# Optimization experiments

Measured on AMD Instinct MI355X. Metric: run time of the kernel, lower is better.

## Reference

```python
import jax, jax.numpy as jnp
import numpy as np

# ---- config (from Mamba2Config defaults) ----
D_MODEL = 1024
D_STATE = 128
D_CONV = 4
EXPAND = 2
HEADDIM = 64
D_INNER = EXPAND * D_MODEL          # 2048
NHEADS = D_INNER // HEADDIM         # 32
CONV_DIM = D_INNER + 2 * D_STATE    # 2304 (ngroups=1)
D_IN_PROJ = 2 * D_INNER + 2 * D_STATE + NHEADS  # 4384
INTER = ((int(D_MODEL * 8 / 3) + 63) // 64) * 64  # 2752
EPS = 1e-6
BATCH, SEQLEN = 2, 1024


def rmsnorm(x, w):
    return x * jax.lax.rsqrt(jnp.mean(x * x, axis=-1, keepdims=True) + EPS) * w


def setup_inputs() -> dict:
    key = jax.random.key(0)
    ks = jax.random.split(key, 16)
    s = 0.02
    return {
        "hidden_states": jax.random.normal(ks[0], (BATCH, SEQLEN, D_MODEL), jnp.float32),
        "norm_w": jnp.ones((D_MODEL,), jnp.float32),
        "in_proj_w": jax.random.normal(ks[1], (D_IN_PROJ, D_MODEL), jnp.float32) * s,
        "conv_w": jax.random.normal(ks[2], (CONV_DIM, D_CONV), jnp.float32) * 0.2,
        "conv_b": jnp.zeros((CONV_DIM,), jnp.float32),
        "dt_bias": jax.random.normal(ks[3], (NHEADS,), jnp.float32) * 0.5,
        "A_log": jnp.log(jax.random.uniform(ks[4], (NHEADS,), jnp.float32, 1.0, 16.0)),
        "D": jnp.ones((NHEADS,), jnp.float32) + jax.random.normal(ks[5], (NHEADS,), jnp.float32) * 0.05,
        "ssm_norm_w": jnp.ones((D_INNER,), jnp.float32),
        "out_proj_w": jax.random.normal(ks[6], (D_MODEL, D_INNER), jnp.float32) * s,
        "post_norm_w": jnp.ones((D_MODEL,), jnp.float32),
        "gate_w": jax.random.normal(ks[7], (INTER, D_MODEL), jnp.float32) * s,
        "up_w": jax.random.normal(ks[8], (INTER, D_MODEL), jnp.float32) * s,
        "down_w": jax.random.normal(ks[9], (D_MODEL, INTER), jnp.float32) * s,
    }


def _mixer(u, in_proj_w, conv_w, conv_b, dt_bias, A_log, D, ssm_norm_w, out_proj_w):
    b, l, _ = u.shape
    zxbcdt = u @ in_proj_w.T                              # (b,l,4384)
    z = zxbcdt[..., :D_INNER]                             # gate
    xBC = zxbcdt[..., D_INNER:D_INNER + CONV_DIM]
    dt = zxbcdt[..., -NHEADS:]

    # causal depthwise conv1d (kernel D_CONV) + SiLU
    xp = jnp.pad(xBC, ((0, 0), (D_CONV - 1, 0), (0, 0)))
    xBC = sum(xp[:, k:k + l, :] * conv_w[:, k] for k in range(D_CONV)) + conv_b
    xBC = jax.nn.silu(xBC)

    xs = xBC[..., :D_INNER].reshape(b, l, NHEADS, HEADDIM)   # (b,l,h,p)
    Bm = xBC[..., D_INNER:D_INNER + D_STATE]                  # (b,l,n)
    Cm = xBC[..., -D_STATE:]                                  # (b,l,n)

    dt = jax.nn.softplus(dt + dt_bias)                        # (b,l,h)
    A = -jnp.exp(A_log)                                       # (h,)

    def step(h, inp):
        dt_t, x_t, B_t, C_t = inp                             # (b,h),(b,h,p),(b,n),(b,n)
        dA = jnp.exp(dt_t * A)                                # (b,h)
        h = h * dA[..., None, None] + jnp.einsum('bh,bhp,bn->bhpn', dt_t, x_t, B_t)
        y_t = jnp.einsum('bhpn,bn->bhp', h, C_t)
        return h, y_t

    h0 = jnp.zeros((b, NHEADS, HEADDIM, D_STATE), u.dtype)
    xsT = (jnp.moveaxis(dt, 1, 0), jnp.moveaxis(xs, 1, 0),
           jnp.moveaxis(Bm, 1, 0), jnp.moveaxis(Cm, 1, 0))
    _, yT = jax.lax.scan(step, h0, xsT)                       # (l,b,h,p)
    y = jnp.moveaxis(yT, 0, 1) + D[None, None, :, None] * xs  # skip term
    y = y.reshape(b, l, D_INNER)

    # gated RMSNorm (norm_before_gate=False): normalize y*silu(z)
    y = rmsnorm(y * jax.nn.silu(z), ssm_norm_w)
    return y @ out_proj_w.T


def reference(hidden_states, norm_w, in_proj_w, conv_w, conv_b, dt_bias, A_log, D,
              ssm_norm_w, out_proj_w, post_norm_w, gate_w, up_w, down_w):
    res = hidden_states
    h = rmsnorm(hidden_states, norm_w)
    h = _mixer(h, in_proj_w, conv_w, conv_b, dt_bias, A_log, D, ssm_norm_w, out_proj_w)
    x = res + h
    res = x
    h = rmsnorm(x, post_norm_w)
    h = (jax.nn.silu(h @ gate_w.T) * (h @ up_w.T)) @ down_w.T  # SwiGLU MLP
    return res + h
```

## Files before the change

### kernel.cpp

```cpp
#include <hip/hip_runtime.h>
#include <hip/hip_bf16.h>

#define SEQLEN   1024
#define NTOK     2048
#define DMODEL   1024
#define DSTATE   128
#define DINNER   2048
#define NHEADS   32
#define HEADDIM  64
#define CONVDIM  2304
#define DINPROJ  4384
#define INTER    2752
#define Q        64
#define NCHUNK   16

typedef __hip_bfloat16 bf16;
typedef unsigned short ushort_t;
typedef __attribute__((ext_vector_type(8))) short bf16x8;
typedef __attribute__((ext_vector_type(4))) float f32x4;
typedef __attribute__((ext_vector_type(4))) unsigned short u16x4;

__device__ __forceinline__ float bf2f(bf16 x) { return __bfloat162float(x); }
__device__ __forceinline__ float bfu2f(ushort_t u) {
    return __uint_as_float(((unsigned)u) << 16);
}
__device__ __forceinline__ ushort_t f2bfu(float x) {
    union { bf16 h; ushort_t u; } c; c.h = __float2bfloat16(x); return c.u;
}

__device__ __forceinline__ void glds16(const void* g, void* l) {
    __builtin_amdgcn_global_load_lds(
        (const __attribute__((address_space(1))) void*)g,
        (__attribute__((address_space(3))) void*)l, 16, 0, 0);
}

__device__ inline float block_reduce_sum(float v) {
    __shared__ float red[4];
    #pragma unroll
    for (int off = 32; off >= 1; off >>= 1) v += __shfl_down(v, off);
    int lane = threadIdx.x & 63, w = threadIdx.x >> 6;
    if (lane == 0) red[w] = v;
    __syncthreads();
    return red[0] + red[1] + red[2] + red[3];
}

__global__ __launch_bounds__(256) void f2bf_kernel(
    const float* __restrict__ src, ushort_t* __restrict__ dst, int n)
{
    const int i = (blockIdx.x * 256 + threadIdx.x) * 4;
    if (i < n) {
        const f32x4 v = *(const f32x4*)(src + i);
        u16x4 o;
        #pragma unroll
        for (int k = 0; k < 4; k++) o[k] = f2bfu(v[k]);
        *(u16x4*)(dst + i) = o;
    }
}

#define NWOP (DMODEL * DINNER)
#define NWG  (INTER * DMODEL)
__global__ __launch_bounds__(256) void convert_weights_kernel(
    const float* __restrict__ wop, const float* __restrict__ wg,
    const float* __restrict__ wu, const float* __restrict__ wd,
    ushort_t* __restrict__ dWop, ushort_t* __restrict__ dWgu,
    ushort_t* __restrict__ dWdn)
{
    const int i4 = (blockIdx.x * 256 + threadIdx.x) * 4;
    const float* src;
    ushort_t* dst;
    if (i4 < NWOP) { src = wop + i4; dst = dWop + i4; }
    else if (i4 < NWOP + NWG) {
        const int e = i4 - NWOP, row = e >> 10, col = e & 1023;
        src = wg + e; dst = dWgu + ((size_t)(2 * row) << 10) + col;
    } else if (i4 < NWOP + 2 * NWG) {
        const int e = i4 - NWOP - NWG, row = e >> 10, col = e & 1023;
        src = wu + e; dst = dWgu + ((size_t)(2 * row + 1) << 10) + col;
    } else if (i4 < NWOP + 3 * NWG) {
        const int e = i4 - NWOP - 2 * NWG;
        src = wd + e; dst = dWdn + e;
    } else return;
    const f32x4 v = *(const f32x4*)src;
    u16x4 o;
    #pragma unroll
    for (int k = 0; k < 4; k++) o[k] = f2bfu(v[k]);
    *(u16x4*)dst = o;
}

__global__ __launch_bounds__(256) void rmsnorm1024_kernel(
    const float* __restrict__ x, const float* __restrict__ w, bf16* __restrict__ out)
{
    const int token = blockIdx.x, t = threadIdx.x;
    float v[4]; float ss = 0.f;
    #pragma unroll
    for (int i = 0; i < 4; i++) {
        v[i] = x[(size_t)token * DMODEL + t * 4 + i];
        ss += v[i] * v[i];
    }
    ss = block_reduce_sum(ss);
    const float scale = rsqrtf(ss * (1.0f / DMODEL) + 1e-6f);
    #pragma unroll
    for (int i = 0; i < 4; i++)
        out[(size_t)token * DMODEL + t * 4 + i] =
            __float2bfloat16(v[i] * scale * w[t * 4 + i]);
}

template <int EPI, int MT, int NT>
__global__ __launch_bounds__(256) void gemm_bf(
    const bf16* __restrict__ A, const bf16* __restrict__ W,
    float* __restrict__ Cf, const float* __restrict__ resid_f,
    bf16* __restrict__ out_bf, int M, int N, int K)
{
    __shared__ ushort_t As[MT * 32];
    __shared__ ushort_t Bs[NT * 32];
    const int tid = threadIdx.x;
    const int w = tid >> 6, lane = tid & 63;
    const int m0 = blockIdx.y * MT, n0 = blockIdx.x * NT;

    const int srow = tid >> 2;
    const int skof = (tid & 3) * 8;
    const bf16* Ag0 = A + (size_t)(m0 + srow) * K + skof;
    const bf16* Ag1 = Ag0 + (size_t)64 * K;
    const int nr0 = n0 + srow, nr1 = n0 + 64 + srow;
    const bf16* Wg0 = W + (size_t)(nr0 < N ? nr0 : 0) * K + skof;
    const bf16* Wg1 = W + (size_t)((NT == 128 && nr1 < N) ? nr1 : 0) * K + skof;
    ushort_t* lA0 = &As[w * 512];
    ushort_t* lA1 = &As[2048 + w * 512];
    ushort_t* lB0 = &Bs[w * 512];
    ushort_t* lB1 = &Bs[2048 + w * 512];

    const int wy = w >> 1, wx = w & 1;
    const int fr = lane & 15;
    const int fk = (lane >> 4) * 8;
    constexpr int MI = MT / 32;
    constexpr int NJ = NT / 32;
    f32x4 acc[MI][NJ];
    #pragma unroll
    for (int i = 0; i < MI; i++)
        #pragma unroll
        for (int j = 0; j < NJ; j++)
            acc[i][j] = (f32x4){0.f, 0.f, 0.f, 0.f};

    for (int k0 = 0; k0 < K; k0 += 32) {
        __syncthreads();
        glds16(Ag0 + k0, lA0);
        if (MT == 128) glds16(Ag1 + k0, lA1);
        glds16(Wg0 + k0, lB0);
        if (NT == 128) glds16(Wg1 + k0, lB1);
        __syncthreads();
        bf16x8 af[MI], bfv[NJ];
        #pragma unroll
        for (int i = 0; i < MI; i++)
            af[i] = *(const bf16x8*)&As[(wy * (MT / 2) + i * 16 + fr) * 32 + fk];
        #pragma unroll
        for (int j = 0; j < NJ; j++)
            bfv[j] = *(const bf16x8*)&Bs[(wx * (NT / 2) + j * 16 + fr) * 32 + fk];
        #pragma unroll
        for (int i = 0; i < MI; i++)
            #pragma unroll
            for (int j = 0; j < NJ; j++)
                acc[i][j] = __builtin_amdgcn_mfma_f32_16x16x32_bf16(
                    af[i], bfv[j], acc[i][j], 0, 0, 0);
    }

    #pragma unroll
    for (int i = 0; i < MI; i++) {
        #pragma unroll
        for (int j = 0; j < NJ; j++) {
            const int mb = m0 + wy * (MT / 2) + i * 16 + (lane >> 4) * 4;
            const int nn = n0 + wx * (NT / 2) + j * 16 + (lane & 15);
            if (nn < N) {
                #pragma unroll
                for (int r = 0; r < 4; r++) {
                    if (EPI == 2) {
                        const float g = acc[i][j][r];
                        const float u = __shfl_xor(g, 1);
                        if (!(lane & 1)) {
                            const float a = (g / (1.f + expf(-g))) * u;
                            out_bf[(size_t)(mb + r) * (N / 2) + (nn >> 1)] =
                                __float2bfloat16(a);
                        }
                    } else {
                        const size_t idx = (size_t)(mb + r) * N + nn;
                        float v = acc[i][j][r];
                        if (EPI == 1) v += resid_f[idx];
                        Cf[idx] = v;
                    }
                }
            }
        }
    }
}

__global__ __launch_bounds__(256) void conv_silu_kernel(
    const float* __restrict__ zx, const float* __restrict__ cw,
    const float* __restrict__ cb, ushort_t* __restrict__ out)
{
    const int idx = blockIdx.x * 256 + threadIdx.x;
    if (idx >= NTOK * CONVDIM) return;
    const int c = idx % CONVDIM;
    const int token = idx / CONVDIM;
    const int l = token & (SEQLEN - 1);
    float acc = cb[c];
    #pragma unroll
    for (int k = 0; k < 4; k++) {
        const int ls = l - 3 + k;
        if (ls >= 0)
            acc += zx[(size_t)(token - 3 + k) * DINPROJ + DINNER + c] * cw[c * 4 + k];
    }
    out[(size_t)token * CONVDIM + c] = f2bfu(acc / (1.f + expf(-acc)));
}

__global__ __launch_bounds__(256) void dt_softplus_kernel(
    const float* __restrict__ zx, const float* __restrict__ dtb,
    float* __restrict__ out)
{
    const int idx = blockIdx.x * 256 + threadIdx.x;
    const int h = idx & (NHEADS - 1);
    const int token = idx >> 5;
    float v = zx[(size_t)token * DINPROJ + (DINNER + CONVDIM) + h] + dtb[h];
    out[idx] = (v > 20.f) ? v : log1pf(expf(v));
}

__global__ __launch_bounds__(256) void chunk_state_kernel(
    const ushort_t* __restrict__ cvb, const float* __restrict__ dtb,
    const float* __restrict__ A_log, float* __restrict__ ccum,
    ushort_t* __restrict__ Sbuf)
{
    const int bx = blockIdx.x;
    const int bh = bx >> 4, c = bx & 15;
    const int b = bh >> 5, h = bh & 31;
    const int t = threadIdx.x;
    const int w = t >> 6, lane = t & 63;
    const int wy = w >> 1, wx = w & 1;
    const int fr = lane & 15, fk = (lane >> 4) * 8, cr = (lane >> 4) * 4;
    const int tok0 = b * SEQLEN + c * Q;
    const float A = -expf(A_log[h]);

    __shared__ ushort_t sXT[64 * 88];
    __shared__ ushort_t sBT[128 * 88];
    __shared__ float sW[64];

    if (t < 64) {
        const float d = dtb[(size_t)(tok0 + t) * NHEADS + h];
        float s = d;
        #pragma unroll
        for (int off = 1; off < 64; off <<= 1) {
            const float up = __shfl_up(s, off);
            if (t >= off) s += up;
        }
        const float total = __shfl(s, 63);
        sW[t] = expf(A * (total - s)) * d;
        if (t == 63) ccum[bh * NCHUNK + c] = A * total;
    }
    __syncthreads();

    for (int i = t; i < 64 * 64; i += 256) {
        const int l = i >> 6, p = i & 63;
        const float v = bfu2f(cvb[(size_t)(tok0 + l) * CONVDIM + h * HEADDIM + p]);
        sXT[p * 88 + l] = f2bfu(sW[l] * v);
    }
    for (int i = t; i < 128 * 64; i += 256) {
        const int l = i >> 7, n = i & 127;
        sBT[n * 88 + l] = cvb[(size_t)(tok0 + l) * CONVDIM + DINNER + n];
    }
    __syncthreads();

    f32x4 acc[2][4];
    #pragma unroll
    for (int i = 0; i < 2; i++)
        #pragma unroll
        for (int j = 0; j < 4; j++)
            acc[i][j] = (f32x4){0.f, 0.f, 0.f, 0.f};
    #pragma unroll
    for (int k0 = 0; k0 < 64; k0 += 32) {
        bf16x8 af[2], bfv[4];
        #pragma unroll
        for (int i = 0; i < 2; i++)
            af[i] = *(const bf16x8*)&sXT[(wy * 32 + i * 16 + fr) * 88 + fk + k0];
        #pragma unroll
        for (int j = 0; j < 4; j++)
            bfv[j] = *(const bf16x8*)&sBT[(wx * 64 + j * 16 + fr) * 88 + fk + k0];
        #pragma unroll
        for (int i = 0; i < 2; i++)
            #pragma unroll
            for (int j = 0; j < 4; j++)
                acc[i][j] = __builtin_amdgcn_mfma_f32_16x16x32_bf16(
                    af[i], bfv[j], acc[i][j], 0, 0, 0);
    }
    const size_t slot = (size_t)(bh * NCHUNK + c) * 64 * 128;
    #pragma unroll
    for (int i = 0; i < 2; i++) {
        #pragma unroll
        for (int j = 0; j < 4; j++) {
            #pragma unroll
            for (int r = 0; r < 4; r++) {
                const int pr = wy * 32 + i * 16 + cr + r;
                const int nn = wx * 64 + j * 16 + fr;
                Sbuf[slot + pr * 128 + nn] = f2bfu(acc[i][j][r]);
            }
        }
    }
}

__global__ __launch_bounds__(256) void stitch_kernel(
    const float* __restrict__ ccum, ushort_t* __restrict__ Sbuf)
{
    const int bh = blockIdx.x;
    const int t = threadIdx.x, p = t >> 2, q = t & 3;
    float H[32];
    #pragma unroll
    for (int j = 0; j < 32; j++) H[j] = 0.f;
    for (int c = 0; c < NCHUNK; c++) {
        const float P = expf(ccum[bh * NCHUNK + c]);
        const size_t slot = ((size_t)(bh * NCHUNK + c) * 64 + p) * 128;
        #pragma unroll
        for (int jj = 0; jj < 8; jj++) {
            const u16x4 sv4 = *(const u16x4*)&Sbuf[slot + q * 4 + 16 * jj];
            u16x4 hv4;
            #pragma unroll
            for (int k = 0; k < 4; k++) hv4[k] = f2bfu(H[jj * 4 + k]);
            *(u16x4*)&Sbuf[slot + q * 4 + 16 * jj] = hv4;
            #pragma unroll
            for (int k = 0; k < 4; k++)
                H[jj * 4 + k] = P * H[jj * 4 + k] + bfu2f(sv4[k]);
        }
    }
}

__global__ __launch_bounds__(256) void chunk_scan_mfma_kernel(
    const ushort_t* __restrict__ cvb, const float* __restrict__ dtb,
    const float* __restrict__ A_log, const float* __restrict__ Dh,
    const ushort_t* __restrict__ Sbuf, bf16* __restrict__ ybuf)
{
    const int bx = blockIdx.x;
    const int bh = bx >> 4, c = bx & 15;
    const int b = bh >> 5, h = bh & 31;
    const int t = threadIdx.x;
    const int w = t >> 6, lane = t & 63;
    const int wy = w >> 1, wx = w & 1;
    const int fr = lane & 15;
    const int fk = (lane >> 4) * 8;
    const int cr = (lane >> 4) * 4;
    const int tok0 = b * SEQLEN + c * Q;
    const float A = -expf(A_log[h]);
    const float Dv = Dh[h];

    __shared__ ushort_t sB[64 * 136];
    __shared__ ushort_t sC[64 * 136];
    __shared__ ushort_t sH[64 * 136];
    __shared__ ushort_t sXT[64 * 72];
    __shared__ ushort_t sM[64 * 72];
    __shared__ float    sCum[64];
    __shared__ float    sDtv[64];

    for (int i = t; i < 64 * 32; i += 256) {
        const int row = i >> 5, col = (i & 31) * 4;
        const size_t base = (size_t)(tok0 + row) * CONVDIM;
        *(u16x4*)&sB[row * 136 + col] = *(const u16x4*)&cvb[base + DINNER + col];
        *(u16x4*)&sC[row * 136 + col] = *(const u16x4*)&cvb[base + DINNER + DSTATE + col];
    }
    for (int i = t; i < 64 * 32; i += 256) {
        const int p = i >> 5, l0 = (i & 31) * 2;
        const ushort_t x0 = cvb[(size_t)(tok0 + l0)     * CONVDIM + h * HEADDIM + p];
        const ushort_t x1 = cvb[(size_t)(tok0 + l0 + 1) * CONVDIM + h * HEADDIM + p];
        *(unsigned*)&sXT[p * 72 + l0] = ((unsigned)x1 << 16) | x0;
    }
    {
        const size_t slot = (size_t)(bh * NCHUNK + c) * 64 * 128;
        for (int i = t * 4; i < 64 * 128; i += 1024) {
            const int row = i >> 7, col = i & 127;
            *(u16x4*)&sH[row * 136 + col] = *(const u16x4*)&Sbuf[slot + row * 128 + col];
        }
    }
    if (t < 64) {
        const float d = dtb[(size_t)(tok0 + t) * NHEADS + h];
        float s = d;
        #pragma unroll
        for (int off = 1; off < 64; off <<= 1) {
            const float up = __shfl_up(s, off);
            if (t >= off) s += up;
        }
        sCum[t] = A * s;
        sDtv[t] = d;
    }
    __syncthreads();

    f32x4 accg[2][2];
    #pragma unroll
    for (int i = 0; i < 2; i++)
        #pragma unroll
        for (int j = 0; j < 2; j++)
            accg[i][j] = (f32x4){0.f, 0.f, 0.f, 0.f};
    #pragma unroll
    for (int k0 = 0; k0 < 128; k0 += 32) {
        bf16x8 af[2], bfv[2];
        #pragma unroll
        for (int i = 0; i < 2; i++)
            af[i] = *(const bf16x8*)&sC[(wy * 32 + i * 16 + fr) * 136 + fk + k0];
        #pragma unroll
        for (int j = 0; j < 2; j++)
            bfv[j] = *(const bf16x8*)&sB[(wx * 32 + j * 16 + fr) * 136 + fk + k0];
        #pragma unroll
        for (int i = 0; i < 2; i++)
            #pragma unroll
            for (int j = 0; j < 2; j++)
                accg[i][j] = __builtin_amdgcn_mfma_f32_16x16x32_bf16(
                    af[i], bfv[j], accg[i][j], 0, 0, 0);
    }
    __syncthreads();

    #pragma unroll
    for (int i = 0; i < 2; i++) {
        #pragma unroll
        for (int j = 0; j < 2; j++) {
            #pragma unroll
            for (int r = 0; r < 4; r++) {
                const int l  = wy * 32 + i * 16 + cr + r;
                const int jc = wx * 32 + j * 16 + fr;
                const float v = (jc <= l)
                    ? accg[i][j][r] * expf(sCum[l] - sCum[jc]) * sDtv[jc] : 0.f;
                sM[l * 72 + jc] = f2bfu(v);
            }
        }
    }
    for (int i = t; i < 64 * 32; i += 256) {
        const int row = i >> 5, col = (i & 31) * 4;
        const float sc = expf(sCum[row]);
        u16x4 v = *(const u16x4*)&sC[row * 136 + col];
        #pragma unroll
        for (int k = 0; k < 4; k++) v[k] = f2bfu(bfu2f(v[k]) * sc);
        *(u16x4*)&sC[row * 136 + col] = v;
    }
    __syncthreads();

    f32x4 accy[2][2];
    #pragma unroll
    for (int i = 0; i < 2; i++)
        #pragma unroll
        for (int j = 0; j < 2; j++)
            accy[i][j] = (f32x4){0.f, 0.f, 0.f, 0.f};
    #pragma unroll
    for (int k0 = 0; k0 < 64; k0 += 32) {
        bf16x8 af[2], bfv[2];
        #pragma unroll
        for (int i = 0; i < 2; i++)
            af[i] = *(const bf16x8*)&sM[(wy * 32 + i * 16 + fr) * 72 + fk + k0];
        #pragma unroll
        for (int j = 0; j < 2; j++)
            bfv[j] = *(const bf16x8*)&sXT[(wx * 32 + j * 16 + fr) * 72 + fk + k0];
        #pragma unroll
        for (int i = 0; i < 2; i++)
            #pragma unroll
            for (int j = 0; j < 2; j++)
                accy[i][j] = __builtin_amdgcn_mfma_f32_16x16x32_bf16(
                    af[i], bfv[j], accy[i][j], 0, 0, 0);
    }
    #pragma unroll
    for (int k0 = 0; k0 < 128; k0 += 32) {
        bf16x8 af[2], bfv[2];
        #pragma unroll
        for (int i = 0; i < 2; i++)
            af[i] = *(const bf16x8*)&sC[(wy * 32 + i * 16 + fr) * 136 + fk + k0];
        #pragma unroll
        for (int j = 0; j < 2; j++)
            bfv[j] = *(const bf16x8*)&sH[(wx * 32 + j * 16 + fr) * 136 + fk + k0];
        #pragma unroll
        for (int i = 0; i < 2; i++)
            #pragma unroll
            for (int j = 0; j < 2; j++)
                accy[i][j] = __builtin_amdgcn_mfma_f32_16x16x32_bf16(
                    af[i], bfv[j], accy[i][j], 0, 0, 0);
    }

    #pragma unroll
    for (int i = 0; i < 2; i++) {
        #pragma unroll
        for (int j = 0; j < 2; j++) {
            #pragma unroll
            for (int r = 0; r < 4; r++) {
                const int l = wy * 32 + i * 16 + cr + r;
                const int p = wx * 32 + j * 16 + fr;
                const float x = bfu2f(sXT[p * 72 + l]);
                ybuf[(size_t)(tok0 + l) * DINNER + h * HEADDIM + p] =
                    __float2bfloat16(accy[i][j][r] + Dv * x);
            }
        }
    }
}

__global__ __launch_bounds__(256) void gated_rmsnorm_kernel(
    const bf16* __restrict__ y, const float* __restrict__ zx,
    const float* __restrict__ w, bf16* __restrict__ out)
{
    const int token = blockIdx.x, t = threadIdx.x;
    const bf16* yr = y + (size_t)token * DINNER;
    const float* zr = zx + (size_t)token * DINPROJ;
    float v[8]; float ss = 0.f;
    #pragma unroll
    for (int i = 0; i < 8; i++) {
        const int idx = t * 8 + i;
        const float zz = zr[idx];
        const float val = bf2f(yr[idx]) * (zz / (1.f + expf(-zz)));
        v[i] = val; ss += val * val;
    }
    ss = block_reduce_sum(ss);
    const float scale = rsqrtf(ss * (1.0f / DINNER) + 1e-6f);
    #pragma unroll
    for (int i = 0; i < 8; i++) {
        const int idx = t * 8 + i;
        out[(size_t)token * DINNER + idx] =
            __float2bfloat16(v[i] * scale * w[idx]);
    }
}

extern "C" void kernel_launch(void* const* d_in, const int* in_sizes, int n_in,
                              void* d_out, int out_size, void* d_ws, size_t ws_size,
                              hipStream_t stream) {
    const float* hidden     = (const float*)d_in[0];
    const float* norm_w     = (const float*)d_in[1];
    const float* in_proj_w  = (const float*)d_in[2];
    const float* conv_w     = (const float*)d_in[3];
    const float* conv_b     = (const float*)d_in[4];
    const float* dt_bias    = (const float*)d_in[5];
    const float* A_log      = (const float*)d_in[6];
    const float* Dh         = (const float*)d_in[7];
    const float* ssm_norm_w = (const float*)d_in[8];
    const float* out_proj_w = (const float*)d_in[9];
    const float* post_norm_w= (const float*)d_in[10];
    const float* gate_w     = (const float*)d_in[11];
    const float* up_w       = (const float*)d_in[12];
    const float* down_w     = (const float*)d_in[13];
    float* out = (float*)d_out;

    float* ws = (float*)d_ws;
    bf16*  h_norm = (bf16*)(ws);
    float* zx     = ws + 1048576;
    ushort_t* cvb = (ushort_t*)(ws + 10027008);
    float* dtb    = ws + 14745600;
    float* ccum   = ws + 14811136;
    ushort_t* Sbuf= (ushort_t*)(ws + 14812160);
    float* xbuf   = ws + 19006464;
    bf16*  ybuf   = (bf16*)(ws + 21103616);
    bf16*  ynorm  = (bf16*)(ws + 22152192);
    ushort_t* Wip = (ushort_t*)(ws + 10027008);
    ushort_t* Wop = (ushort_t*)(ws + 1048576);
    ushort_t* Wgu = (ushort_t*)(ws + 2097152);
    ushort_t* Wdn = (ushort_t*)(ws + 4915200);
    bf16*  act    = (bf16*)(ws + 6324224);
    bf16*  h2     = h_norm;

    f2bf_kernel<<<4384, 256, 0, stream>>>(in_proj_w, Wip, DINPROJ * DMODEL);
    rmsnorm1024_kernel<<<NTOK, 256, 0, stream>>>(hidden, norm_w, h_norm);
    gemm_bf<0, 128, 128><<<dim3(35, 16), 256, 0, stream>>>(h_norm, (const bf16*)Wip, zx,
        nullptr, nullptr, NTOK, DINPROJ, DMODEL);
    conv_silu_kernel<<<(NTOK * CONVDIM) / 256, 256, 0, stream>>>(zx, conv_w, conv_b, cvb);
    dt_softplus_kernel<<<(NTOK * NHEADS) / 256, 256, 0, stream>>>(zx, dt_bias, dtb);
    chunk_state_kernel<<<1024, 256, 0, stream>>>(cvb, dtb, A_log, ccum, Sbuf);
    stitch_kernel<<<64, 256, 0, stream>>>(ccum, Sbuf);
    chunk_scan_mfma_kernel<<<1024, 256, 0, stream>>>(cvb, dtb, A_log, Dh, Sbuf, ybuf);
    gated_rmsnorm_kernel<<<NTOK, 256, 0, stream>>>(ybuf, zx, ssm_norm_w, ynorm);
    convert_weights_kernel<<<(NWOP + 3 * NWG) / 1024, 256, 0, stream>>>(
        out_proj_w, gate_w, up_w, down_w, Wop, Wgu, Wdn);
    gemm_bf<1, 64, 64><<<dim3(16, 32), 256, 0, stream>>>(ynorm, (const bf16*)Wop, xbuf,
        hidden, nullptr, NTOK, DMODEL, DINNER);
    rmsnorm1024_kernel<<<NTOK, 256, 0, stream>>>(xbuf, post_norm_w, h2);
    gemm_bf<2, 128, 128><<<dim3(43, 16), 256, 0, stream>>>(h2, (const bf16*)Wgu,
        nullptr, nullptr, act, NTOK, 2 * INTER, DMODEL);
    gemm_bf<1, 64, 64><<<dim3(16, 32), 256, 0, stream>>>(act, (const bf16*)Wdn, out,
        xbuf, nullptr, NTOK, DMODEL, INTER);
}
```

Baseline: 378.1 us.

## Double GEMM K-tile to 64 and XOR-swizzle LDS layout

```diff
diff --git a/kernel.cpp b/kernel.cpp
--- a/kernel.cpp
+++ b/kernel.cpp
@@ -110,27 +110,30 @@
     float* __restrict__ Cf, const float* __restrict__ resid_f,
     bf16* __restrict__ out_bf, int M, int N, int K)
 {
-    __shared__ ushort_t As[MT * 32];
-    __shared__ ushort_t Bs[NT * 32];
+    __shared__ ushort_t As[MT * 64];
+    __shared__ ushort_t Bs[NT * 64];
     const int tid = threadIdx.x;
     const int w = tid >> 6, lane = tid & 63;
     const int m0 = blockIdx.y * MT, n0 = blockIdx.x * NT;
 
-    const int srow = tid >> 2;
-    const int skof = (tid & 3) * 8;
-    const bf16* Ag0 = A + (size_t)(m0 + srow) * K + skof;
-    const bf16* Ag1 = Ag0 + (size_t)64 * K;
-    const int nr0 = n0 + srow, nr1 = n0 + 64 + srow;
-    const bf16* Wg0 = W + (size_t)(nr0 < N ? nr0 : 0) * K + skof;
-    const bf16* Wg1 = W + (size_t)((NT == 128 && nr1 < N) ? nr1 : 0) * K + skof;
-    ushort_t* lA0 = &As[w * 512];
-    ushort_t* lA1 = &As[2048 + w * 512];
-    ushort_t* lB0 = &Bs[w * 512];
-    ushort_t* lB1 = &Bs[2048 + w * 512];
+    const int srow = tid >> 3;
+    const int scol = (((tid & 7) ^ (srow & 7)) * 8);
+    const bf16* Agp[MT / 32];
+    const bf16* Wgp[NT / 32];
+    #pragma unroll
+    for (int i = 0; i < MT / 32; i++)
+        Agp[i] = A + (size_t)(m0 + i * 32 + srow) * K + scol;
+    #pragma unroll
+    for (int i = 0; i < NT / 32; i++) {
+        const int nr = n0 + i * 32 + srow;
+        Wgp[i] = W + (size_t)(nr < N ? nr : 0) * K + scol;
+    }
+    ushort_t* lA = &As[w * 512];
+    ushort_t* lB = &Bs[w * 512];
 
     const int wy = w >> 1, wx = w & 1;
     const int fr = lane & 15;
-    const int fk = (lane >> 4) * 8;
+    const int fq = lane >> 4;
     constexpr int MI = MT / 32;
     constexpr int NJ = NT / 32;
     f32x4 acc[MI][NJ];
@@ -140,26 +143,37 @@
         for (int j = 0; j < NJ; j++)
             acc[i][j] = (f32x4){0.f, 0.f, 0.f, 0.f};
 
-    for (int k0 = 0; k0 < K; k0 += 32) {
+    for (int k0 = 0; k0 < K; k0 += 64) {
         __syncthreads();
-        glds16(Ag0 + k0, lA0);
-        if (MT == 128) glds16(Ag1 + k0, lA1);
-        glds16(Wg0 + k0, lB0);
-        if (NT == 128) glds16(Wg1 + k0, lB1);
+        #pragma unroll
+        for (int i = 0; i < MT / 32; i++)
+            glds16(Agp[i] + k0, lA + i * 2048);
+        #pragma unroll
+        for (int i = 0; i < NT / 32; i++)
+            glds16(Wgp[i] + k0, lB + i * 2048);
         __syncthreads();
-        bf16x8 af[MI], bfv[NJ];
-        #pragma unroll
-        for (int i = 0; i < MI; i++)
-            af[i] = *(const bf16x8*)&As[(wy * (MT / 2) + i * 16 + fr) * 32 + fk];
-        #pragma unroll
-        for (int j = 0; j < NJ; j++)
-            bfv[j] = *(const bf16x8*)&Bs[(wx * (NT / 2) + j * 16 + fr) * 32 + fk];
-        #pragma unroll
-        for (int i = 0; i < MI; i++)
-            #pragma unroll
-            for (int j = 0; j < NJ; j++)
-                acc[i][j] = __builtin_amdgcn_mfma_f32_16x16x32_bf16(
-                    af[i], bfv[j], acc[i][j], 0, 0, 0);
+        #pragma unroll
+        for (int ks = 0; ks < 2; ks++) {
+            bf16x8 af[MI], bfv[NJ];
+            #pragma unroll
+            for (int i = 0; i < MI; i++) {
+                const int r = wy * (MT / 2) + i * 16 + fr;
+                const int g = ks * 4 + fq;
+                af[i] = *(const bf16x8*)&As[r * 64 + ((g ^ (r & 7)) * 8)];
+            }
+            #pragma unroll
+            for (int j = 0; j < NJ; j++) {
+                const int r = wx * (NT / 2) + j * 16 + fr;
+                const int g = ks * 4 + fq;
+                bfv[j] = *(const bf16x8*)&Bs[r * 64 + ((g ^ (r & 7)) * 8)];
+            }
+            #pragma unroll
+            for (int i = 0; i < MI; i++)
+                #pragma unroll
+                for (int j = 0; j < NJ; j++)
+                    acc[i][j] = __builtin_amdgcn_mfma_f32_16x16x32_bf16(
+                        af[i], bfv[j], acc[i][j], 0, 0, 0);
+        }
     }
 
     #pragma unroll
```

Measured after the change: 372.9 us. No clear change (-1.4%).
